# Kernel optimization log

Measured on AMD Instinct MI355X. Metric: run time of the kernel, lower is better.

## Reference

```python
import jax, jax.numpy as jnp
import numpy as np


def setup_inputs() -> dict:
    key = jax.random.key(0)
    k1, k2 = jax.random.split(key)
    B, Sx, Sy, D = 8, 2048, 2048, 1024
    x = jax.random.normal(k1, (B, Sx, D), dtype=jnp.float32)
    y = jax.random.normal(k2, (B, Sy, D), dtype=jnp.float32)
    return {"x": x, "y": y}


def reference(x, y):
    # e[b,i,j] = x[b,i,:] . y[b,j,:]  (UNscaled, as in the original)
    e = jnp.einsum('bid,bjd->bij', x, y)
    ai = jax.nn.softmax(e, axis=-1)
    # a[b,i,:] = sum_j ai[b,i,j] * y[b,j,:]
    a = jnp.einsum('bij,bjd->bid', ai, y)
    # concat along feature dim; dropout p=0 -> identity
    out = jnp.concatenate([x, a], axis=-1)  # [B, Sx, 2D]
    return out
```

## Files before the change

kernel.cpp:

```cpp
#include <hip/hip_runtime.h>
#include <stdint.h>

#define SX 2048
#define SYY 2048
#define DDIM 1024
#define NBATCH 8

typedef _Float16 f16;
typedef __attribute__((ext_vector_type(4))) _Float16 h4_t;
typedef __attribute__((ext_vector_type(8))) _Float16 h8_t;
typedef __attribute__((ext_vector_type(4))) float fx4_t;

__device__ __forceinline__ void gload_lds16(const void* g, void* l) {
  __builtin_amdgcn_global_load_lds((const __attribute__((address_space(1))) void*)g,
                                   (__attribute__((address_space(3))) void*)l,
                                   16, 0, 0);
}

__global__ __launch_bounds__(256) void k_prep_x(const float4* __restrict__ x,
                                                float* __restrict__ out,
                                                h4_t* __restrict__ x16, long n4) {
  long i = (long)blockIdx.x * blockDim.x + threadIdx.x;
  long stride = (long)gridDim.x * blockDim.x;
  for (; i < n4; i += stride) {
    long bi = i >> 8;
    int dq = (int)(i & 255);
    float4 v = x[i];
    *(float4*)(out + bi * (2 * DDIM) + dq * 4) = v;
    h4_t h = { (f16)v.x, (f16)v.y, (f16)v.z, (f16)v.w };
    x16[i] = h;
  }
}

__global__ __launch_bounds__(256) void k_trans(const float* __restrict__ y,
                                               f16* __restrict__ y16,
                                               f16* __restrict__ yt16) {
  __shared__ f16 tile[64][72];
  int z = blockIdx.z;
  int d0 = blockIdx.x * 64, j0 = blockIdx.y * 64;
  const float* yb = y + (size_t)z * SYY * DDIM;
  f16* y16b = y16 + (size_t)z * SYY * DDIM;
  f16* ytb = yt16 + (size_t)z * DDIM * SYY;
  int t = threadIdx.x;
  int jl = t >> 2;
  int dq = t & 3;
#pragma unroll
  for (int s = 0; s < 4; ++s) {
    int dl = dq * 16 + s * 4;
    float4 v = *(const float4*)(yb + (size_t)(j0 + jl) * DDIM + d0 + dl);
    h4_t h = { (f16)v.x, (f16)v.y, (f16)v.z, (f16)v.w };
    *(h4_t*)(y16b + (size_t)(j0 + jl) * DDIM + d0 + dl) = h;
    *(h4_t*)&tile[jl][dl] = h;
  }
  __syncthreads();
  int dl2 = t >> 2;
  int jq = t & 3;
  f16 vbuf[16] __attribute__((aligned(16)));
#pragma unroll
  for (int u = 0; u < 16; ++u) vbuf[u] = tile[jq * 16 + u][dl2];
  f16* orow = ytb + (size_t)(d0 + dl2) * SYY + j0 + jq * 16;
  *(uint4*)orow = *(const uint4*)&vbuf[0];
  *(uint4*)(orow + 8) = *(const uint4*)&vbuf[8];
}

#define PH_BAR() __builtin_amdgcn_s_barrier()

#define STAGE_A(SLOT, HALF, T) {                                               \
    const f16* s_ = aRow + (size_t)((HALF) * 64) * lda + (T) * 64;             \
    f16* d_ = lds + (SLOT) * 8192 + dstoff;                                    \
    gload_lds16(s_, d_);                                                       \
    gload_lds16(s_ + (size_t)128 * lda, d_ + 4096); }

#define STAGE_B(SLOT, HALF, T) {                                               \
    const f16* s_ = bRow + (size_t)((HALF) * 32) * ldb + (T) * 64;             \
    f16* d_ = lds + (SLOT) * 8192 + dstoff;                                    \
    gload_lds16(s_, d_);                                                       \
    gload_lds16(s_ + (size_t)128 * ldb, d_ + 4096); }

#define RD_A(PTR, CB) { _Pragma("unroll") for (int i_ = 0; i_ < 4; ++i_) {     \
    af[i_][0] = *(const h8_t*)((PTR) + (CB) + i_ * 2048 + kb0);                \
    af[i_][1] = *(const h8_t*)((PTR) + (CB) + i_ * 2048 + kb1); } }

#define RD_B(PTR, CB, NH) { _Pragma("unroll") for (int j_ = 0; j_ < 2; ++j_) { \
    bf[(NH) + j_][0] = *(const h8_t*)((PTR) + (CB) + j_ * 2048 + kb0);         \
    bf[(NH) + j_][1] = *(const h8_t*)((PTR) + (CB) + j_ * 2048 + kb1); } }

#define MM(MH, NH) { __builtin_amdgcn_s_setprio(1);                            \
  _Pragma("unroll") for (int i_ = 0; i_ < 4; ++i_)                             \
  _Pragma("unroll") for (int j_ = 0; j_ < 2; ++j_) {                           \
    acc[(MH) + i_][(NH) + j_] = __builtin_amdgcn_mfma_f32_16x16x32_f16(        \
        af[i_][0], bf[(NH) + j_][0], acc[(MH) + i_][(NH) + j_], 0, 0, 0);      \
    acc[(MH) + i_][(NH) + j_] = __builtin_amdgcn_mfma_f32_16x16x32_f16(        \
        af[i_][1], bf[(NH) + j_][1], acc[(MH) + i_][(NH) + j_], 0, 0, 0); }    \
  __builtin_amdgcn_s_setprio(0); }

__global__ __launch_bounds__(512, 2) void k_gemm8(
    const f16* __restrict__ A, long a_zs, int a_row0, int lda,
    const f16* __restrict__ B, long b_zs, int ldb,
    float* __restrict__ C, long c_zs, int c_row0, int ldc, int c_col0,
    int K, int ntm, int ntn, int nblk)
{
  __shared__ f16 lds[65536];

  int bid = blockIdx.x;
  int id = bid;
  if ((nblk & 7) == 0) {
    int cpx = nblk >> 3;
    id = (bid & 7) * cpx + (bid >> 3);
  }
  int tpz = ntm * ntn;
  int z = id / tpz;
  int rem = id - z * tpz;
  int mt = rem / ntn;
  int ntl = rem - mt * ntn;
  int m0 = mt * 256, n0 = ntl * 256;

  const int tid = threadIdx.x;
  const int lane = tid & 63, w = tid >> 6;
  const int wr = w >> 2, wc = w & 3;
  const int fr = lane & 15, fh = lane >> 4;

  const f16* Ab = A + (size_t)z * a_zs + (size_t)(a_row0 + m0) * lda;
  const f16* Bb = B + (size_t)z * b_zs + (size_t)n0 * ldb;

  const int l0 = 8 * w + (lane >> 3);
  const int r0a = l0;
  const int r0b = ((l0 >> 5) << 6) | (l0 & 31);
  const int swz = 8 * ((lane & 7) ^ (lane >> 3));
  const f16* aRow = Ab + (size_t)r0a * lda + swz;
  const f16* bRow = Bb + (size_t)r0b * ldb + swz;
  const int dstoff = w * 512 + lane * 8;

  const char* ldsAlo = (const char*)lds + wr * 8192 + fr * 128;
  const char* ldsAhi = ldsAlo + 16384;
  const char* ldsBlo = (const char*)lds + 32768 + wc * 4096 + fr * 128;
  const char* ldsBhi = ldsBlo + 16384;
  const int kb0 = ((0 + fh) ^ (fr & 7)) * 16;
  const int kb1 = ((4 + fh) ^ (fr & 7)) * 16;

  const int nt = K >> 6;
  const int ng = nt >> 1;

  fx4_t acc[8][4];
#pragma unroll
  for (int i = 0; i < 8; ++i)
#pragma unroll
    for (int j = 0; j < 4; ++j) {
      fx4_t zv = {0.f, 0.f, 0.f, 0.f};
      acc[i][j] = zv;
    }
  h8_t af[4][2], bf[4][2];

  STAGE_A(0, 0, 0); STAGE_A(1, 1, 0); STAGE_B(2, 0, 0); STAGE_B(3, 1, 0);
  STAGE_A(4, 0, 1); STAGE_B(6, 0, 1); STAGE_B(7, 1, 1);
  asm volatile("s_waitcnt vmcnt(6)" ::: "memory");
  PH_BAR();

  for (int g = 0; g < ng; ++g) {
    const int T1 = 2 * g + 1, T2 = 2 * g + 2, T3 = 2 * g + 3;
    const bool nl = (g < ng - 1);
    RD_A(ldsAlo, 0); RD_B(ldsBlo, 0, 0);
    STAGE_A(5, 1, T1);
    PH_BAR();
    MM(0, 0);
    PH_BAR();
    RD_B(ldsBhi, 0, 2);
    if (nl) STAGE_A(0, 0, T2);
    PH_BAR();
    MM(0, 2);
    PH_BAR();
    RD_A(ldsAhi, 0);
    if (nl) STAGE_B(2, 0, T2);
    PH_BAR();
    MM(4, 0);
    PH_BAR();
    if (nl) STAGE_B(3, 1, T2);
    PH_BAR();
    MM(4, 2);
    if (nl) { asm volatile("s_waitcnt vmcnt(6)" ::: "memory"); }
    else    { asm volatile("s_waitcnt vmcnt(0)" ::: "memory"); }
    PH_BAR();
    RD_A(ldsAlo, 65536); RD_B(ldsBlo, 65536, 0);
    if (nl) STAGE_A(1, 1, T2);
    PH_BAR();
    MM(0, 0);
    PH_BAR();
    RD_B(ldsBhi, 65536, 2);
    if (nl) STAGE_A(4, 0, T3);
    PH_BAR();
    MM(0, 2);
    PH_BAR();
    RD_A(ldsAhi, 65536);
    if (nl) STAGE_B(6, 0, T3);
    PH_BAR();
    MM(4, 0);
    PH_BAR();
    if (nl) STAGE_B(7, 1, T3);
    PH_BAR();
    MM(4, 2);
    asm volatile("s_waitcnt vmcnt(6)" ::: "memory");
    PH_BAR();
  }

  float* Cb = C + (size_t)z * c_zs +
              (size_t)(c_row0 + m0 + wr * 128) * ldc + c_col0 + n0 + wc * 64;
#pragma unroll
  for (int mi = 0; mi < 8; ++mi)
#pragma unroll
    for (int ni = 0; ni < 4; ++ni)
#pragma unroll
      for (int r = 0; r < 4; ++r)
        Cb[(size_t)(mi * 16 + fh * 4 + r) * ldc + ni * 16 + fr] = acc[mi][ni][r];
}

__global__ __launch_bounds__(256) void k_softmax(const float* __restrict__ S,
                                                 f16* __restrict__ P, long nrows) {
  int wv = threadIdx.x >> 6;
  int lane = threadIdx.x & 63;
  long R = (long)blockIdx.x * 4 + wv;
  if (R >= nrows) return;
  const float* srow = S + R * SYY;
  f16* prow = P + R * SYY;
  float v[32];
#pragma unroll
  for (int c = 0; c < 4; ++c) {
    float4 a = *(const float4*)(srow + c * 512 + lane * 8);
    float4 b = *(const float4*)(srow + c * 512 + lane * 8 + 4);
    v[c * 8 + 0] = a.x; v[c * 8 + 1] = a.y; v[c * 8 + 2] = a.z; v[c * 8 + 3] = a.w;
    v[c * 8 + 4] = b.x; v[c * 8 + 5] = b.y; v[c * 8 + 6] = b.z; v[c * 8 + 7] = b.w;
  }
  float m = v[0];
#pragma unroll
  for (int i = 1; i < 32; ++i) m = fmaxf(m, v[i]);
#pragma unroll
  for (int off = 32; off > 0; off >>= 1) m = fmaxf(m, __shfl_xor(m, off));
  float l = 0.f;
#pragma unroll
  for (int i = 0; i < 32; ++i) { v[i] = __expf(v[i] - m); l += v[i]; }
#pragma unroll
  for (int off = 32; off > 0; off >>= 1) l += __shfl_xor(l, off);
  float r = 1.0f / l;
  f16 h[32] __attribute__((aligned(16)));
#pragma unroll
  for (int i = 0; i < 32; ++i) h[i] = (f16)(v[i] * r);
#pragma unroll
  for (int c = 0; c < 4; ++c)
    *(uint4*)(prow + c * 512 + lane * 8) = *(const uint4*)&h[c * 8];
}

extern "C" void kernel_launch(void* const* d_in, const int* in_sizes, int n_in,
                              void* d_out, int out_size, void* d_ws, size_t ws_size,
                              hipStream_t stream) {
  (void)in_sizes; (void)n_in; (void)out_size;
  const float* x = (const float*)d_in[0];
  const float* y = (const float*)d_in[1];
  float* out = (float*)d_out;

  size_t per_batch = (size_t)SX * SYY * 4 + (size_t)SX * SYY * 2 +
                     (size_t)SX * DDIM * 2 + (size_t)SYY * DDIM * 2 +
                     (size_t)DDIM * SYY * 2;
  int nb = (int)(ws_size / per_batch);
  if (nb > NBATCH) nb = NBATCH;
  int CH = SX;
  if (nb < 1) {
    nb = 1;
    size_t conv = (size_t)SX * DDIM * 2 + (size_t)SYY * DDIM * 2 +
                  (size_t)DDIM * SYY * 2;
    size_t avail = ws_size > conv ? ws_size - conv : 0;
    long ch = (long)(avail / ((size_t)SYY * 6));
    ch = (ch / 256) * 256;
    if (ch < 256) ch = 256;
    if (ch > SX) ch = SX;
    CH = (int)ch;
  }

  char* w = (char*)d_ws;
  float* Sbuf = (float*)w;
  size_t off = (size_t)nb * CH * SYY * 4;
  f16* Pbuf = (f16*)(w + off); off += (size_t)nb * CH * SYY * 2;
  f16* X16 = (f16*)(w + off);  off += (size_t)nb * SX * DDIM * 2;
  f16* Y16 = (f16*)(w + off);  off += (size_t)nb * SYY * DDIM * 2;
  f16* Yt16 = (f16*)(w + off);

  for (int b0 = 0; b0 < NBATCH; b0 += nb) {
    int nbc = (NBATCH - b0 < nb) ? (NBATCH - b0) : nb;
    k_prep_x<<<2048, 256, 0, stream>>>(
        (const float4*)(x + (size_t)b0 * SX * DDIM),
        out + (size_t)b0 * SX * 2 * DDIM, (h4_t*)X16,
        (long)nbc * SX * (DDIM / 4));
    dim3 tg(DDIM / 64, SYY / 64, nbc);
    k_trans<<<tg, 256, 0, stream>>>(y + (size_t)b0 * SYY * DDIM, Y16, Yt16);

    for (int i0 = 0; i0 < SX; i0 += CH) {
      int ntm = CH / 256;
      int nblk1 = nbc * ntm * (SYY / 256);
      k_gemm8<<<nblk1, 512, 0, stream>>>(X16, (long)SX * DDIM, i0, DDIM,
                                         Y16, (long)SYY * DDIM, DDIM,
                                         Sbuf, (long)CH * SYY, 0, SYY, 0,
                                         DDIM, ntm, SYY / 256, nblk1);
      long nrows = (long)nbc * CH;
      k_softmax<<<(unsigned)((nrows + 3) / 4), 256, 0, stream>>>(Sbuf, Pbuf, nrows);
      int nblk2 = nbc * ntm * (DDIM / 256);
      k_gemm8<<<nblk2, 512, 0, stream>>>(Pbuf, (long)CH * SYY, 0, SYY,
                                         Yt16, (long)DDIM * SYY, SYY,
                                         out + (size_t)b0 * SX * 2 * DDIM,
                                         (long)SX * 2 * DDIM, i0, 2 * DDIM, DDIM,
                                         SYY, ntm, DDIM / 256, nblk2);
    }
  }
}
```

Measured before the change: 238.4 us.

## Shrink GEMM tile to 128x256 with K=32 triple-buffered LDS pipeline

Rewrites the fp16 MFMA GEMM to use a 128x256 output tile and a 32-wide K step instead of 256x256 with a 64-wide step. LDS staging becomes a three-slot rotating buffer with a simpler swizzle, LDS use drops to about 72 KB, and launch bounds ask for more resident waves. The intent is to raise occupancy and block count so memory latency is better hidden. The cost is lower arithmetic intensity per tile, more global and LDS traffic per FLOP, and more barriers per unit of work.

```diff
diff --git a/kernel.cpp b/kernel.cpp
--- a/kernel.cpp
+++ b/kernel.cpp
@@ -65,42 +65,32 @@
 
 #define PH_BAR() __builtin_amdgcn_s_barrier()
 
-#define STAGE_A(SLOT, HALF, T) {                                               \
-    const f16* s_ = aRow + (size_t)((HALF) * 64) * lda + (T) * 64;             \
-    f16* d_ = lds + (SLOT) * 8192 + dstoff;                                    \
-    gload_lds16(s_, d_);                                                       \
-    gload_lds16(s_ + (size_t)128 * lda, d_ + 4096); }
-
-#define STAGE_B(SLOT, HALF, T) {                                               \
-    const f16* s_ = bRow + (size_t)((HALF) * 32) * ldb + (T) * 64;             \
-    f16* d_ = lds + (SLOT) * 8192 + dstoff;                                    \
-    gload_lds16(s_, d_);                                                       \
-    gload_lds16(s_ + (size_t)128 * ldb, d_ + 4096); }
-
-#define RD_A(PTR, CB) { _Pragma("unroll") for (int i_ = 0; i_ < 4; ++i_) {     \
-    af[i_][0] = *(const h8_t*)((PTR) + (CB) + i_ * 2048 + kb0);                \
-    af[i_][1] = *(const h8_t*)((PTR) + (CB) + i_ * 2048 + kb1); } }
-
-#define RD_B(PTR, CB, NH) { _Pragma("unroll") for (int j_ = 0; j_ < 2; ++j_) { \
-    bf[(NH) + j_][0] = *(const h8_t*)((PTR) + (CB) + j_ * 2048 + kb0);         \
-    bf[(NH) + j_][1] = *(const h8_t*)((PTR) + (CB) + j_ * 2048 + kb1); } }
-
-#define MM(MH, NH) { __builtin_amdgcn_s_setprio(1);                            \
-  _Pragma("unroll") for (int i_ = 0; i_ < 4; ++i_)                             \
-  _Pragma("unroll") for (int j_ = 0; j_ < 2; ++j_) {                           \
-    acc[(MH) + i_][(NH) + j_] = __builtin_amdgcn_mfma_f32_16x16x32_f16(        \
-        af[i_][0], bf[(NH) + j_][0], acc[(MH) + i_][(NH) + j_], 0, 0, 0);      \
-    acc[(MH) + i_][(NH) + j_] = __builtin_amdgcn_mfma_f32_16x16x32_f16(        \
-        af[i_][1], bf[(NH) + j_][1], acc[(MH) + i_][(NH) + j_], 0, 0, 0); }    \
+#define STAGE_A(SOFF, T) gload_lds16(aSrc + (size_t)(T) * 32, (char*)lds + (SOFF) + adst)
+#define STAGE_B(SOFF, T) {                                                     \
+    gload_lds16(bSrc + (size_t)(T) * 32, (char*)lds + (SOFF) + bdst);          \
+    gload_lds16(bSrc2 + (size_t)(T) * 32, (char*)lds + (SOFF) + 8192 + bdst); }
+
+#define RD_A2(SOFF, M0) {                                                      \
+    af[(M0)]     = *(const h8_t*)(ldsb + (SOFF) + ardoff + (M0) * 1024);       \
+    af[(M0) + 1] = *(const h8_t*)(ldsb + (SOFF) + ardoff + ((M0) + 1) * 1024); }
+
+#define RD_B4(SOFF) { _Pragma("unroll") for (int j_ = 0; j_ < 4; ++j_)         \
+    bf[j_] = *(const h8_t*)(ldsb + (SOFF) + brdoff + j_ * 1024); }
+
+#define MMH(M0) { __builtin_amdgcn_s_setprio(1);                               \
+  _Pragma("unroll") for (int i_ = 0; i_ < 2; ++i_)                             \
+  _Pragma("unroll") for (int j_ = 0; j_ < 4; ++j_)                             \
+    acc[(M0) + i_][j_] = __builtin_amdgcn_mfma_f32_16x16x32_f16(               \
+        af[(M0) + i_], bf[j_], acc[(M0) + i_][j_], 0, 0, 0);                   \
   __builtin_amdgcn_s_setprio(0); }
 
-__global__ __launch_bounds__(512, 2) void k_gemm8(
+__global__ __launch_bounds__(512, 4) void k_gemm8(
     const f16* __restrict__ A, long a_zs, int a_row0, int lda,
     const f16* __restrict__ B, long b_zs, int ldb,
     float* __restrict__ C, long c_zs, int c_row0, int ldc, int c_col0,
     int K, int ntm, int ntn, int nblk)
 {
-  __shared__ f16 lds[65536];
+  __shared__ f16 lds[36864];
 
   int bid = blockIdx.x;
   int id = bid;
@@ -113,7 +103,7 @@
   int rem = id - z * tpz;
   int mt = rem / ntn;
   int ntl = rem - mt * ntn;
-  int m0 = mt * 256, n0 = ntl * 256;
+  int m0 = mt * 128, n0 = ntl * 256;
 
   const int tid = threadIdx.x;
   const int lane = tid & 63, w = tid >> 6;
@@ -123,89 +113,60 @@
   const f16* Ab = A + (size_t)z * a_zs + (size_t)(a_row0 + m0) * lda;
   const f16* Bb = B + (size_t)z * b_zs + (size_t)n0 * ldb;
 
-  const int l0 = 8 * w + (lane >> 3);
-  const int r0a = l0;
-  const int r0b = ((l0 >> 5) << 6) | (l0 & 31);
-  const int swz = 8 * ((lane & 7) ^ (lane >> 3));
-  const f16* aRow = Ab + (size_t)r0a * lda + swz;
-  const f16* bRow = Bb + (size_t)r0b * ldb + swz;
-  const int dstoff = w * 512 + lane * 8;
-
-  const char* ldsAlo = (const char*)lds + wr * 8192 + fr * 128;
-  const char* ldsAhi = ldsAlo + 16384;
-  const char* ldsBlo = (const char*)lds + 32768 + wc * 4096 + fr * 128;
-  const char* ldsBhi = ldsBlo + 16384;
-  const int kb0 = ((0 + fh) ^ (fr & 7)) * 16;
-  const int kb1 = ((4 + fh) ^ (fr & 7)) * 16;
-
-  const int nt = K >> 6;
-  const int ng = nt >> 1;
-
-  fx4_t acc[8][4];
-#pragma unroll
-  for (int i = 0; i < 8; ++i)
+  const int arow = tid >> 2;
+  const int kx = (tid & 3) ^ ((arow >> 1) & 3);
+  const f16* aSrc = Ab + (size_t)arow * lda + kx * 8;
+  const f16* bSrc = Bb + (size_t)arow * ldb + kx * 8;
+  const f16* bSrc2 = bSrc + (size_t)128 * ldb;
+  const int adst = tid * 16;
+  const int bdst = tid * 16;
+
+  const char* ldsb = (const char*)lds;
+  const int voff = fr * 64 + ((fh ^ ((fr >> 1) & 3)) * 16);
+  const int ardoff = wr * 4096 + voff;
+  const int brdoff = wc * 4096 + voff;
+
+  const int nt = K >> 5;
+
+  fx4_t acc[4][4];
+#pragma unroll
+  for (int i = 0; i < 4; ++i)
 #pragma unroll
     for (int j = 0; j < 4; ++j) {
       fx4_t zv = {0.f, 0.f, 0.f, 0.f};
       acc[i][j] = zv;
     }
-  h8_t af[4][2], bf[4][2];
-
-  STAGE_A(0, 0, 0); STAGE_A(1, 1, 0); STAGE_B(2, 0, 0); STAGE_B(3, 1, 0);
-  STAGE_A(4, 0, 1); STAGE_B(6, 0, 1); STAGE_B(7, 1, 1);
-  asm volatile("s_waitcnt vmcnt(6)" ::: "memory");
+  h8_t af[4], bf[4];
+
+  int sa0 = 0, sa1 = 8192, sa2 = 16384;
+  int sb0 = 24576, sb1 = 40960, sb2 = 57344;
+
+  STAGE_A(sa0, 0); STAGE_A(sa1, 1);
+  STAGE_B(sb0, 0); STAGE_B(sb1, 1); STAGE_B(sb2, 2);
+  asm volatile("s_waitcnt vmcnt(4)" ::: "memory");
   PH_BAR();
 
-  for (int g = 0; g < ng; ++g) {
-    const int T1 = 2 * g + 1, T2 = 2 * g + 2, T3 = 2 * g + 3;
-    const bool nl = (g < ng - 1);
-    RD_A(ldsAlo, 0); RD_B(ldsBlo, 0, 0);
-    STAGE_A(5, 1, T1);
-    PH_BAR();
-    MM(0, 0);
-    PH_BAR();
-    RD_B(ldsBhi, 0, 2);
-    if (nl) STAGE_A(0, 0, T2);
-    PH_BAR();
-    MM(0, 2);
-    PH_BAR();
-    RD_A(ldsAhi, 0);
-    if (nl) STAGE_B(2, 0, T2);
-    PH_BAR();
-    MM(4, 0);
-    PH_BAR();
-    if (nl) STAGE_B(3, 1, T2);
-    PH_BAR();
-    MM(4, 2);
-    if (nl) { asm volatile("s_waitcnt vmcnt(6)" ::: "memory"); }
-    else    { asm volatile("s_waitcnt vmcnt(0)" ::: "memory"); }
-    PH_BAR();
-    RD_A(ldsAlo, 65536); RD_B(ldsBlo, 65536, 0);
-    if (nl) STAGE_A(1, 1, T2);
-    PH_BAR();
-    MM(0, 0);
-    PH_BAR();
-    RD_B(ldsBhi, 65536, 2);
-    if (nl) STAGE_A(4, 0, T3);
-    PH_BAR();
-    MM(0, 2);
-    PH_BAR();
-    RD_A(ldsAhi, 65536);
-    if (nl) STAGE_B(6, 0, T3);
-    PH_BAR();
-    MM(4, 0);
-    PH_BAR();
-    if (nl) STAGE_B(7, 1, T3);
-    PH_BAR();
-    MM(4, 2);
-    asm volatile("s_waitcnt vmcnt(6)" ::: "memory");
-    PH_BAR();
+  for (int t = 0; t < nt; ++t) {
+    RD_A2(sa0, 0); RD_B4(sb0);
+    if (t + 2 < nt) STAGE_A(sa2, t + 2);
+    PH_BAR();
+    MMH(0);
+    PH_BAR();
+    RD_A2(sa0, 2);
+    if (t + 3 < nt) STAGE_B(sb0, t + 3);
+    PH_BAR();
+    MMH(2);
+    if (t < nt - 3) { asm volatile("s_waitcnt vmcnt(5)" ::: "memory"); }
+    else            { asm volatile("s_waitcnt vmcnt(0)" ::: "memory"); }
+    PH_BAR();
+    int ta = sa0; sa0 = sa1; sa1 = sa2; sa2 = ta;
+    int tb = sb0; sb0 = sb1; sb1 = sb2; sb2 = tb;
   }
 
   float* Cb = C + (size_t)z * c_zs +
-              (size_t)(c_row0 + m0 + wr * 128) * ldc + c_col0 + n0 + wc * 64;
-#pragma unroll
-  for (int mi = 0; mi < 8; ++mi)
+              (size_t)(c_row0 + m0 + wr * 64) * ldc + c_col0 + n0 + wc * 64;
+#pragma unroll
+  for (int mi = 0; mi < 4; ++mi)
 #pragma unroll
     for (int ni = 0; ni < 4; ++ni)
 #pragma unroll
@@ -292,7 +253,7 @@
     k_trans<<<tg, 256, 0, stream>>>(y + (size_t)b0 * SYY * DDIM, Y16, Yt16);
 
     for (int i0 = 0; i0 < SX; i0 += CH) {
-      int ntm = CH / 256;
+      int ntm = CH / 128;
       int nblk1 = nbc * ntm * (SYY / 256);
       k_gemm8<<<nblk1, 512, 0, stream>>>(X16, (long)SX * DDIM, i0, DDIM,
                                          Y16, (long)SYY * DDIM, DDIM,
```

Result: slower. 261.5 us (+9.7%).

## Fuse split softmax into first GEMM epilogue and rescale rows in second GEMM

Applied to the files above, without the earlier changes.

The first GEMM now computes a per-tile softmax in its epilogue. It finds each row's max and sum across the four wave columns through LDS, stores unnormalized exponentials as fp16, and writes the per-tile (max, sum) pairs. A small kernel merges the eight tile statistics per row into fp16 correction factors. The second GEMM multiplies its A fragments by those factors as it reads them from LDS. This removes the fp32 score buffer and the separate softmax pass, and tile ordering is also changed. The cost is extra VALU work in the inner loop of the second GEMM, and fp16 scaling that may lose precision for rows whose tile maxima differ widely.

```diff
diff --git a/kernel.cpp b/kernel.cpp
--- a/kernel.cpp
+++ b/kernel.cpp
@@ -7,6 +7,7 @@
 #define NBATCH 8
 
 typedef _Float16 f16;
+typedef __attribute__((ext_vector_type(2))) _Float16 h2_t;
 typedef __attribute__((ext_vector_type(4))) _Float16 h4_t;
 typedef __attribute__((ext_vector_type(8))) _Float16 h8_t;
 typedef __attribute__((ext_vector_type(4))) float fx4_t;
@@ -81,6 +82,14 @@
     af[i_][0] = *(const h8_t*)((PTR) + (CB) + i_ * 2048 + kb0);                \
     af[i_][1] = *(const h8_t*)((PTR) + (CB) + i_ * 2048 + kb1); } }
 
+#define RD_A_S(PTR, CB, MOFF) { _Pragma("unroll") for (int i_ = 0; i_ < 4; ++i_) { \
+    h8_t a0 = *(const h8_t*)((PTR) + (CB) + i_ * 2048 + kb0);                  \
+    h8_t a1 = *(const h8_t*)((PTR) + (CB) + i_ * 2048 + kb1);                  \
+    h2_t* p0 = (h2_t*)&a0; h2_t* p1 = (h2_t*)&a1;                              \
+    _Pragma("unroll") for (int q_ = 0; q_ < 4; ++q_) {                         \
+      p0[q_] *= fdc[(MOFF) + i_]; p1[q_] *= fdc[(MOFF) + i_]; }                \
+    af[i_][0] = a0; af[i_][1] = a1; } }
+
 #define RD_B(PTR, CB, NH) { _Pragma("unroll") for (int j_ = 0; j_ < 2; ++j_) { \
     bf[(NH) + j_][0] = *(const h8_t*)((PTR) + (CB) + j_ * 2048 + kb0);         \
     bf[(NH) + j_][1] = *(const h8_t*)((PTR) + (CB) + j_ * 2048 + kb1); } }
@@ -94,49 +103,52 @@
         af[i_][1], bf[(NH) + j_][1], acc[(MH) + i_][(NH) + j_], 0, 0, 0); }    \
   __builtin_amdgcn_s_setprio(0); }
 
-__global__ __launch_bounds__(512, 2) void k_gemm8(
+#define DECODE_TILE()                                                          \
+  int bid = blockIdx.x;                                                        \
+  int id = bid;                                                                \
+  if ((nblk & 7) == 0) { int cpx = nblk >> 3; id = (bid & 7) * cpx + (bid >> 3); } \
+  int tpz = ntm * ntn;                                                         \
+  int z = id / tpz;                                                            \
+  int rem = id - z * tpz;                                                      \
+  int mt, ntl;                                                                 \
+  if ((ntm & 1) == 0) {                                                        \
+    int ht = tpz >> 1, hm = ntm >> 1;                                          \
+    int half = rem / ht, j = rem - half * ht;                                  \
+    ntl = j / hm; mt = half * hm + (j - ntl * hm);                             \
+  } else { mt = rem / ntn; ntl = rem - mt * ntn; }                             \
+  int m0 = mt * 256, n0 = ntl * 256;
+
+#define GEMM_COMMON_SETUP()                                                    \
+  const int tid = threadIdx.x;                                                 \
+  const int lane = tid & 63, w = tid >> 6;                                     \
+  const int wr = w >> 2, wc = w & 3;                                           \
+  const int fr = lane & 15, fh = lane >> 4;                                    \
+  const f16* Ab = A + (size_t)z * a_zs + (size_t)(a_row0 + m0) * lda;          \
+  const f16* Bb = B + (size_t)z * b_zs + (size_t)n0 * ldb;                     \
+  const int l0 = 8 * w + (lane >> 3);                                          \
+  const int r0a = l0;                                                          \
+  const int r0b = ((l0 >> 5) << 6) | (l0 & 31);                                \
+  const int swz = 8 * ((lane & 7) ^ (lane >> 3));                              \
+  const f16* aRow = Ab + (size_t)r0a * lda + swz;                              \
+  const f16* bRow = Bb + (size_t)r0b * ldb + swz;                              \
+  const int dstoff = w * 512 + lane * 8;                                       \
+  const char* ldsAlo = (const char*)lds + wr * 8192 + fr * 128;                \
+  const char* ldsAhi = ldsAlo + 16384;                                         \
+  const char* ldsBlo = (const char*)lds + 32768 + wc * 4096 + fr * 128;        \
+  const char* ldsBhi = ldsBlo + 16384;                                         \
+  const int kb0 = ((0 + fh) ^ (fr & 7)) * 16;                                  \
+  const int kb1 = ((4 + fh) ^ (fr & 7)) * 16;
+
+__global__ __launch_bounds__(512, 2) void k_gemm1(
     const f16* __restrict__ A, long a_zs, int a_row0, int lda,
     const f16* __restrict__ B, long b_zs, int ldb,
-    float* __restrict__ C, long c_zs, int c_row0, int ldc, int c_col0,
+    f16* __restrict__ U, long u_zs,
+    float2* __restrict__ ML, int mrows,
     int K, int ntm, int ntn, int nblk)
 {
   __shared__ f16 lds[65536];
-
-  int bid = blockIdx.x;
-  int id = bid;
-  if ((nblk & 7) == 0) {
-    int cpx = nblk >> 3;
-    id = (bid & 7) * cpx + (bid >> 3);
-  }
-  int tpz = ntm * ntn;
-  int z = id / tpz;
-  int rem = id - z * tpz;
-  int mt = rem / ntn;
-  int ntl = rem - mt * ntn;
-  int m0 = mt * 256, n0 = ntl * 256;
-
-  const int tid = threadIdx.x;
-  const int lane = tid & 63, w = tid >> 6;
-  const int wr = w >> 2, wc = w & 3;
-  const int fr = lane & 15, fh = lane >> 4;
-
-  const f16* Ab = A + (size_t)z * a_zs + (size_t)(a_row0 + m0) * lda;
-  const f16* Bb = B + (size_t)z * b_zs + (size_t)n0 * ldb;
-
-  const int l0 = 8 * w + (lane >> 3);
-  const int r0a = l0;
-  const int r0b = ((l0 >> 5) << 6) | (l0 & 31);
-  const int swz = 8 * ((lane & 7) ^ (lane >> 3));
-  const f16* aRow = Ab + (size_t)r0a * lda + swz;
-  const f16* bRow = Bb + (size_t)r0b * ldb + swz;
-  const int dstoff = w * 512 + lane * 8;
-
-  const char* ldsAlo = (const char*)lds + wr * 8192 + fr * 128;
-  const char* ldsAhi = ldsAlo + 16384;
-  const char* ldsBlo = (const char*)lds + 32768 + wc * 4096 + fr * 128;
-  const char* ldsBhi = ldsBlo + 16384;
-  const int kb0 = ((0 + fh) ^ (fr & 7)) * 16;
-  const int kb1 = ((4 + fh) ^ (fr & 7)) * 16;
+  DECODE_TILE();
+  GEMM_COMMON_SETUP();
 
   const int nt = K >> 6;
   const int ng = nt >> 1;
@@ -145,10 +157,7 @@
 #pragma unroll
   for (int i = 0; i < 8; ++i)
 #pragma unroll
-    for (int j = 0; j < 4; ++j) {
-      fx4_t zv = {0.f, 0.f, 0.f, 0.f};
-      acc[i][j] = zv;
-    }
+    for (int j = 0; j < 4; ++j) { fx4_t zv = {0.f,0.f,0.f,0.f}; acc[i][j] = zv; }
   h8_t af[4][2], bf[4][2];
 
   STAGE_A(0, 0, 0); STAGE_A(1, 1, 0); STAGE_B(2, 0, 0); STAGE_B(3, 1, 0);
@@ -202,6 +211,207 @@
     PH_BAR();
   }
 
+  __syncthreads();
+  float* red = (float*)lds;
+  const int rbase = wr * 128 + fh * 4;
+  float pm[8][4];
+#pragma unroll
+  for (int mi = 0; mi < 8; ++mi)
+#pragma unroll
+    for (int rr = 0; rr < 4; ++rr)
+      pm[mi][rr] = fmaxf(fmaxf(acc[mi][0][rr], acc[mi][1][rr]),
+                         fmaxf(acc[mi][2][rr], acc[mi][3][rr]));
+#pragma unroll
+  for (int off = 8; off > 0; off >>= 1)
+#pragma unroll
+    for (int mi = 0; mi < 8; ++mi)
+#pragma unroll
+      for (int rr = 0; rr < 4; ++rr)
+        pm[mi][rr] = fmaxf(pm[mi][rr], __shfl_xor(pm[mi][rr], off));
+  if (fr == 0)
+#pragma unroll
+    for (int mi = 0; mi < 8; ++mi)
+#pragma unroll
+      for (int rr = 0; rr < 4; ++rr)
+        red[wc * 256 + rbase + mi * 16 + rr] = pm[mi][rr];
+  __syncthreads();
+  float mrow[8][4];
+#pragma unroll
+  for (int mi = 0; mi < 8; ++mi)
+#pragma unroll
+    for (int rr = 0; rr < 4; ++rr) {
+      int r = rbase + mi * 16 + rr;
+      mrow[mi][rr] = fmaxf(fmaxf(red[r], red[256 + r]),
+                           fmaxf(red[512 + r], red[768 + r]));
+    }
+  __syncthreads();
+  float ps[8][4];
+#pragma unroll
+  for (int mi = 0; mi < 8; ++mi)
+#pragma unroll
+    for (int rr = 0; rr < 4; ++rr) {
+      float s = 0.f;
+#pragma unroll
+      for (int ni = 0; ni < 4; ++ni) {
+        float e = __expf(acc[mi][ni][rr] - mrow[mi][rr]);
+        acc[mi][ni][rr] = e;
+        s += e;
+      }
+      ps[mi][rr] = s;
+    }
+#pragma unroll
+  for (int off = 8; off > 0; off >>= 1)
+#pragma unroll
+    for (int mi = 0; mi < 8; ++mi)
+#pragma unroll
+      for (int rr = 0; rr < 4; ++rr)
+        ps[mi][rr] += __shfl_xor(ps[mi][rr], off);
+  if (fr == 0)
+#pragma unroll
+    for (int mi = 0; mi < 8; ++mi)
+#pragma unroll
+      for (int rr = 0; rr < 4; ++rr)
+        red[wc * 256 + rbase + mi * 16 + rr] = ps[mi][rr];
+  __syncthreads();
+  f16* Ub = U + (size_t)z * u_zs;
+#pragma unroll
+  for (int mi = 0; mi < 8; ++mi)
+#pragma unroll
+    for (int ni = 0; ni < 4; ++ni)
+#pragma unroll
+      for (int rr = 0; rr < 4; ++rr)
+        Ub[(size_t)(m0 + rbase + mi * 16 + rr) * SYY +
+           n0 + wc * 64 + ni * 16 + fr] = (f16)acc[mi][ni][rr];
+  if (wc == 0 && fr == 0) {
+    float2* MLp = ML + ((size_t)z * 8 + ntl) * mrows + m0;
+#pragma unroll
+    for (int mi = 0; mi < 8; ++mi)
+#pragma unroll
+      for (int rr = 0; rr < 4; ++rr) {
+        int r = rbase + mi * 16 + rr;
+        float l4 = red[r] + red[256 + r] + red[512 + r] + red[768 + r];
+        float2 v; v.x = mrow[mi][rr]; v.y = l4;
+        MLp[r] = v;
+      }
+  }
+}
+
+__global__ __launch_bounds__(256) void k_mlred(const float2* __restrict__ ML,
+                                               f16* __restrict__ Fq,
+                                               int rows, long total) {
+  long idx = (long)blockIdx.x * blockDim.x + threadIdx.x;
+  if (idx >= total) return;
+  int z = (int)(idx / rows);
+  int r = (int)(idx - (long)z * rows);
+  float2 v[8];
+  float M = -3.4e38f;
+#pragma unroll
+  for (int t = 0; t < 8; ++t) {
+    v[t] = ML[((size_t)z * 8 + t) * rows + r];
+    M = fmaxf(M, v[t].x);
+  }
+  float L = 0.f;
+#pragma unroll
+  for (int t = 0; t < 8; ++t) L += v[t].y * __expf(v[t].x - M);
+  float inv = 1.0f / L;
+#pragma unroll
+  for (int t = 0; t < 8; ++t)
+    Fq[((size_t)z * 8 + t) * rows + r] = (f16)(__expf(v[t].x - M) * inv);
+}
+
+__global__ __launch_bounds__(512, 2) void k_gemm2(
+    const f16* __restrict__ A, long a_zs, int a_row0, int lda,
+    const f16* __restrict__ B, long b_zs, int ldb,
+    float* __restrict__ C, long c_zs, int c_row0, int ldc, int c_col0,
+    const f16* __restrict__ Fq, int mrows,
+    int K, int ntm, int ntn, int nblk)
+{
+  __shared__ f16 lds[65536];
+  DECODE_TILE();
+  GEMM_COMMON_SETUP();
+
+  const int nt = K >> 6;
+  const int ng = nt >> 1;
+
+  fx4_t acc[8][4];
+#pragma unroll
+  for (int i = 0; i < 8; ++i)
+#pragma unroll
+    for (int j = 0; j < 4; ++j) { fx4_t zv = {0.f,0.f,0.f,0.f}; acc[i][j] = zv; }
+  h8_t af[4][2], bf[4][2];
+
+  const f16* Fb = Fq + (size_t)z * 8 * mrows + m0 + wr * 128 + fr;
+  h2_t fdc[8], fdn[8];
+#pragma unroll
+  for (int i = 0; i < 8; ++i) {
+    f16 fv = Fb[i * 16];
+    h2_t d; d[0] = fv; d[1] = fv; fdn[i] = d;
+  }
+
+  STAGE_A(0, 0, 0); STAGE_A(1, 1, 0); STAGE_B(2, 0, 0); STAGE_B(3, 1, 0);
+  STAGE_A(4, 0, 1); STAGE_B(6, 0, 1); STAGE_B(7, 1, 1);
+  asm volatile("s_waitcnt vmcnt(6)" ::: "memory");
+  PH_BAR();
+
+  for (int g = 0; g < ng; ++g) {
+    const int T1 = 2 * g + 1, T2 = 2 * g + 2, T3 = 2 * g + 3;
+    const bool nl = (g < ng - 1);
+    if ((g & 1) == 0) {
+#pragma unroll
+      for (int i = 0; i < 8; ++i) fdc[i] = fdn[i];
+      int tn = (g >> 1) + 1;
+      if (tn < 8) {
+        const f16* Fn = Fb + (size_t)tn * mrows;
+#pragma unroll
+        for (int i = 0; i < 8; ++i) {
+          f16 fv = Fn[i * 16];
+          h2_t d; d[0] = fv; d[1] = fv; fdn[i] = d;
+        }
+      }
+    }
+    RD_A_S(ldsAlo, 0, 0); RD_B(ldsBlo, 0, 0);
+    STAGE_A(5, 1, T1);
+    PH_BAR();
+    MM(0, 0);
+    PH_BAR();
+    RD_B(ldsBhi, 0, 2);
+    if (nl) STAGE_A(0, 0, T2);
+    PH_BAR();
+    MM(0, 2);
+    PH_BAR();
+    RD_A_S(ldsAhi, 0, 4);
+    if (nl) STAGE_B(2, 0, T2);
+    PH_BAR();
+    MM(4, 0);
+    PH_BAR();
+    if (nl) STAGE_B(3, 1, T2);
+    PH_BAR();
+    MM(4, 2);
+    if (nl) { asm volatile("s_waitcnt vmcnt(6)" ::: "memory"); }
+    else    { asm volatile("s_waitcnt vmcnt(0)" ::: "memory"); }
+    PH_BAR();
+    RD_A_S(ldsAlo, 65536, 0); RD_B(ldsBlo, 65536, 0);
+    if (nl) STAGE_A(1, 1, T2);
+    PH_BAR();
+    MM(0, 0);
+    PH_BAR();
+    RD_B(ldsBhi, 65536, 2);
+    if (nl) STAGE_A(4, 0, T3);
+    PH_BAR();
+    MM(0, 2);
+    PH_BAR();
+    RD_A_S(ldsAhi, 65536, 4);
+    if (nl) STAGE_B(6, 0, T3);
+    PH_BAR();
+    MM(4, 0);
+    PH_BAR();
+    if (nl) STAGE_B(7, 1, T3);
+    PH_BAR();
+    MM(4, 2);
+    asm volatile("s_waitcnt vmcnt(6)" ::: "memory");
+    PH_BAR();
+  }
+
   float* Cb = C + (size_t)z * c_zs +
               (size_t)(c_row0 + m0 + wr * 128) * ldc + c_col0 + n0 + wc * 64;
 #pragma unroll
@@ -211,41 +421,6 @@
 #pragma unroll
       for (int r = 0; r < 4; ++r)
         Cb[(size_t)(mi * 16 + fh * 4 + r) * ldc + ni * 16 + fr] = acc[mi][ni][r];
-}
-
-__global__ __launch_bounds__(256) void k_softmax(const float* __restrict__ S,
-                                                 f16* __restrict__ P, long nrows) {
-  int wv = threadIdx.x >> 6;
-  int lane = threadIdx.x & 63;
-  long R = (long)blockIdx.x * 4 + wv;
-  if (R >= nrows) return;
-  const float* srow = S + R * SYY;
-  f16* prow = P + R * SYY;
-  float v[32];
-#pragma unroll
-  for (int c = 0; c < 4; ++c) {
-    float4 a = *(const float4*)(srow + c * 512 + lane * 8);
-    float4 b = *(const float4*)(srow + c * 512 + lane * 8 + 4);
-    v[c * 8 + 0] = a.x; v[c * 8 + 1] = a.y; v[c * 8 + 2] = a.z; v[c * 8 + 3] = a.w;
-    v[c * 8 + 4] = b.x; v[c * 8 + 5] = b.y; v[c * 8 + 6] = b.z; v[c * 8 + 7] = b.w;
-  }
-  float m = v[0];
-#pragma unroll
-  for (int i = 1; i < 32; ++i) m = fmaxf(m, v[i]);
-#pragma unroll
-  for (int off = 32; off > 0; off >>= 1) m = fmaxf(m, __shfl_xor(m, off));
-  float l = 0.f;
-#pragma unroll
-  for (int i = 0; i < 32; ++i) { v[i] = __expf(v[i] - m); l += v[i]; }
-#pragma unroll
-  for (int off = 32; off > 0; off >>= 1) l += __shfl_xor(l, off);
-  float r = 1.0f / l;
-  f16 h[32] __attribute__((aligned(16)));
-#pragma unroll
-  for (int i = 0; i < 32; ++i) h[i] = (f16)(v[i] * r);
-#pragma unroll
-  for (int c = 0; c < 4; ++c)
-    *(uint4*)(prow + c * 512 + lane * 8) = *(const uint4*)&h[c * 8];
 }
 
 extern "C" void kernel_launch(void* const* d_in, const int* in_sizes, int n_in,
@@ -256,7 +431,7 @@
   const float* y = (const float*)d_in[1];
   float* out = (float*)d_out;
 
-  size_t per_batch = (size_t)SX * SYY * 4 + (size_t)SX * SYY * 2 +
+  size_t per_batch = (size_t)SX * SYY * 2 + (size_t)8 * SX * 8 + (size_t)8 * SX * 2 +
                      (size_t)SX * DDIM * 2 + (size_t)SYY * DDIM * 2 +
                      (size_t)DDIM * SYY * 2;
   int nb = (int)(ws_size / per_batch);
@@ -267,7 +442,7 @@
     size_t conv = (size_t)SX * DDIM * 2 + (size_t)SYY * DDIM * 2 +
                   (size_t)DDIM * SYY * 2;
     size_t avail = ws_size > conv ? ws_size - conv : 0;
-    long ch = (long)(avail / ((size_t)SYY * 6));
+    long ch = (long)(avail / ((size_t)SYY * 2 + 80));
     ch = (ch / 256) * 256;
     if (ch < 256) ch = 256;
     if (ch > SX) ch = SX;
@@ -275,11 +450,11 @@
   }
 
   char* w = (char*)d_ws;
-  float* Sbuf = (float*)w;
-  size_t off = (size_t)nb * CH * SYY * 4;
-  f16* Pbuf = (f16*)(w + off); off += (size_t)nb * CH * SYY * 2;
-  f16* X16 = (f16*)(w + off);  off += (size_t)nb * SX * DDIM * 2;
-  f16* Y16 = (f16*)(w + off);  off += (size_t)nb * SYY * DDIM * 2;
+  f16* Ubuf = (f16*)w;            size_t off = (size_t)nb * CH * SYY * 2;
+  float2* MLbuf = (float2*)(w + off); off += (size_t)nb * 8 * CH * 8;
+  f16* Fqbuf = (f16*)(w + off);   off += (size_t)nb * 8 * CH * 2;
+  f16* X16 = (f16*)(w + off);     off += (size_t)nb * SX * DDIM * 2;
+  f16* Y16 = (f16*)(w + off);     off += (size_t)nb * SYY * DDIM * 2;
   f16* Yt16 = (f16*)(w + off);
 
   for (int b0 = 0; b0 < NBATCH; b0 += nb) {
@@ -294,17 +469,20 @@
     for (int i0 = 0; i0 < SX; i0 += CH) {
       int ntm = CH / 256;
       int nblk1 = nbc * ntm * (SYY / 256);
-      k_gemm8<<<nblk1, 512, 0, stream>>>(X16, (long)SX * DDIM, i0, DDIM,
+      k_gemm1<<<nblk1, 512, 0, stream>>>(X16, (long)SX * DDIM, i0, DDIM,
                                          Y16, (long)SYY * DDIM, DDIM,
-                                         Sbuf, (long)CH * SYY, 0, SYY, 0,
+                                         Ubuf, (long)CH * SYY,
+                                         MLbuf, CH,
                                          DDIM, ntm, SYY / 256, nblk1);
-      long nrows = (long)nbc * CH;
-      k_softmax<<<(unsigned)((nrows + 3) / 4), 256, 0, stream>>>(Sbuf, Pbuf, nrows);
+      long rows_total = (long)nbc * CH;
+      k_mlred<<<(unsigned)((rows_total + 255) / 256), 256, 0, stream>>>(
+          MLbuf, Fqbuf, CH, rows_total);
       int nblk2 = nbc * ntm * (DDIM / 256);
-      k_gemm8<<<nblk2, 512, 0, stream>>>(Pbuf, (long)CH * SYY, 0, SYY,
+      k_gemm2<<<nblk2, 512, 0, stream>>>(Ubuf, (long)CH * SYY, 0, SYY,
                                          Yt16, (long)DDIM * SYY, SYY,
                                          out + (size_t)b0 * SX * 2 * DDIM,
                                          (long)SX * 2 * DDIM, i0, 2 * DDIM, DDIM,
+                                         Fqbuf, CH,
                                          SYY, ntm, DDIM / 256, nblk2);
     }
   }
```

Result: faster. 221.0 us (-7.3%).
